# Kernel optimization log

Hardware: AMD Instinct MI355X
Metric: run time of the kernel (lower is better)

## Reference

```python
import jax, jax.numpy as jnp
import numpy as np

IN_DIM = 1024
HID = 256
OUT_DIM = 1000
NUM_BINS = 51
BATCH = 2048
N_LEGAL = 200


def setup_inputs() -> dict:
    key = jax.random.key(0)
    ks = jax.random.split(key, 12)
    s = lambda fan_in: 1.0 / np.sqrt(fan_in)
    u = lambda k, shp, b: jax.random.uniform(k, shp, jnp.float32, -b, b)
    return {
        "x": jax.random.normal(ks[0], (BATCH, IN_DIM), jnp.float32),
        # weights stored as [in, out] (math-equivalent to torch Linear)
        "w_in": u(ks[1], (IN_DIM, HID), s(IN_DIM)),
        "b_in": u(ks[2], (HID,), s(IN_DIM)),
        "w_ah": u(ks[3], (HID, HID), s(HID)),
        "b_ah": u(ks[4], (HID,), s(HID)),
        "w_ao": u(ks[5], (HID, OUT_DIM * NUM_BINS), s(HID)),
        "b_ao": u(ks[6], (OUT_DIM * NUM_BINS,), s(HID)),
        "w_vh": u(ks[7], (HID, HID), s(HID)),
        "b_vh": u(ks[8], (HID,), s(HID)),
        "w_vo": u(ks[9], (HID, NUM_BINS), s(HID)),
        "b_vo": u(ks[10], (NUM_BINS,), s(HID)),
        "v_range": jnp.linspace(-10.0, 10.0, NUM_BINS, dtype=jnp.float32),
        "possible_moves": jax.random.randint(ks[11], (BATCH, N_LEGAL), 0, OUT_DIM),
    }


def reference(x, w_in, b_in, w_ah, b_ah, w_ao, b_ao, w_vh, b_vh, w_vo, b_vo,
              v_range, possible_moves):
    B = x.shape[0]
    h = jax.nn.relu(x @ w_in + b_in)                       # [B, 256]
    adv_h = jax.nn.relu(h @ w_ah + b_ah)                   # [B, 256]
    val_h = jax.nn.relu(h @ w_vh + b_vh)                   # [B, 256]
    adv = (adv_h @ w_ao + b_ao).reshape(B, OUT_DIM, NUM_BINS)
    val = (val_h @ w_vo + b_vo).reshape(B, 1, NUM_BINS)
    q = val + adv - adv.mean(axis=1, keepdims=True)        # [B, A, bins]
    p = jnp.maximum(jax.nn.softmax(q, axis=2), 1e-5)       # softmax + clamp(min=1e-5)
    q_vals = jnp.sum(p * v_range, axis=2)                  # [B, A]
    # LegalSoftmax: per-row scatter of 1.0 at legal indices, vectorized
    mask = jnp.zeros((B, OUT_DIM), x.dtype).at[
        jnp.arange(B)[:, None], possible_moves].set(1.0)
    filtered = q_vals * mask
    # faithful to torch: any exact-zero entry (masked OR coincidental) -> -inf
    return jnp.where(filtered == 0, -jnp.inf, filtered)
```

## Files before the change

kernel.cpp:

```cpp
#include <hip/hip_runtime.h>
#include <cstdint>
#include <cstddef>

#define NB      2048
#define INDIM   1024
#define HID     256
#define NA      1000
#define BINS    51
#define NLEG    200
#define NPAIR   (NB*NLEG)
#define NBLK    256
#define PPB     (NPAIR/NBLK)

#define NEG_SENTINEL (-1.0e30f)

typedef float    f32x4  __attribute__((ext_vector_type(4)));
typedef __bf16   bf16x8 __attribute__((ext_vector_type(8)));
typedef unsigned short us8 __attribute__((ext_vector_type(8)));
typedef unsigned short us4 __attribute__((ext_vector_type(4)));
typedef unsigned long long u64x2 __attribute__((ext_vector_type(2)));

__device__ __forceinline__ unsigned short f2bf(float f) {
  union { float f; unsigned u; } v; v.f = f;
  return (unsigned short)((v.u + 0x7FFFu + ((v.u >> 16) & 1u)) >> 16);
}
__device__ __forceinline__ float bf2f(unsigned short h) {
  union { unsigned u; float f; } v; v.u = ((unsigned)h) << 16;
  return v.f;
}
__device__ __forceinline__ bf16x8 as_bf(us8 v) { return __builtin_bit_cast(bf16x8, v); }
__device__ __forceinline__ int imin(int a, int b) { return a < b ? a : b; }

__device__ __forceinline__ unsigned f2fp8x4(float a, float b, float c, float d) {
  int v = 0;
  v = __builtin_amdgcn_cvt_pk_fp8_f32(a, b, v, false);
  v = __builtin_amdgcn_cvt_pk_fp8_f32(c, d, v, true);
  return (unsigned)v;
}
__device__ __forceinline__ unsigned char f2fp8(float f) {
  int v = __builtin_amdgcn_cvt_pk_fp8_f32(f, 0.f, 0, false);
  return (unsigned char)(v & 0xff);
}
__device__ __forceinline__ float fp82f(unsigned char u) {
  return __builtin_amdgcn_cvt_f32_fp8((int)u, 0);
}

__global__ __launch_bounds__(256) void k_phase1(
    const float* __restrict__ w_ao, unsigned char* __restrict__ wp8,
    float* __restrict__ wmean_acc,
    const float* __restrict__ w_in, const float* __restrict__ w_ah,
    const float* __restrict__ w_vh,
    unsigned short* __restrict__ w_inT, unsigned short* __restrict__ w_ahT,
    unsigned short* __restrict__ w_vhT,
    float* __restrict__ out, const int* __restrict__ pm,
    int* __restrict__ hist, int* __restrict__ cnt,
    const float* __restrict__ x, unsigned short* __restrict__ x_bf) {
  __shared__ __align__(16) char smem[26240];
  int b = blockIdx.x, tid = threadIdx.x;
  if (b < 1000) {
    unsigned char* st = (unsigned char*)smem;
    int s = b & 7, a0 = (b >> 3) * 8;
    const float* wbase = w_ao + (size_t)(s * 32) * (NA * BINS) + a0 * BINS;
    for (int i = tid; i < 32 * 102; i += 256) {
      int r = i / 102, c4 = i - r * 102;
      float4 f = *(const float4*)(wbase + (size_t)r * (NA * BINS) + c4 * 4);
      *(unsigned*)(st + r * 420 + c4 * 4) =
          f2fp8x4(f.x * 16.f, f.y * 16.f, f.z * 16.f, f.w * 16.f);
    }
    __syncthreads();
    for (int i = tid; i < 32 * 51; i += 256) {
      int r = i / 51, j = i - r * 51;
      float s8 = 0.f;
#pragma unroll
      for (int aL = 0; aL < 8; aL++) s8 += fp82f(st[r * 420 + aL * 51 + j]);
      atomicAdd(&wmean_acc[(size_t)(s * 32 + r) * BINS + j], s8);
    }
    int t4 = (tid >> 6) & 3, l = tid & 63;
    int col = t4 * 16 + (l & 15), kg = l >> 4;
    for (int aL = 0; aL < 8; aL++) {
      unsigned lo = 0, hi = 0;
      if (col < BINS) {
        const unsigned char* p0 = st + (kg * 8) * 420 + aL * 51 + col;
        lo = (unsigned)p0[0] | ((unsigned)p0[420] << 8) |
             ((unsigned)p0[840] << 16) | ((unsigned)p0[1260] << 24);
        hi = (unsigned)p0[1680] | ((unsigned)p0[2100] << 8) |
             ((unsigned)p0[2520] << 16) | ((unsigned)p0[2940] << 24);
      }
      size_t fg = ((size_t)(a0 + aL) * 8 + s) * 4 + t4;
      uint2 v; v.x = lo; v.y = hi;
      *(uint2*)(wp8 + fg * 512 + (size_t)l * 8) = v;
    }
  } else if (b < 1884) {
    int bb = b - 1000;
    if (bb < 384) {
      float (*tile)[33] = (float(*)[33])smem;
      const float* w; unsigned short* wT; int K, N, kt, nt;
      if (bb < 256)      { w = w_in; wT = w_inT; K = INDIM; N = HID; kt = bb & 31;        nt = bb >> 5; }
      else if (bb < 320) { w = w_ah; wT = w_ahT; K = HID;   N = HID; kt = (bb - 256) & 7; nt = (bb - 256) >> 3; }
      else               { w = w_vh; wT = w_vhT; K = HID;   N = HID; kt = (bb - 320) & 7; nt = (bb - 320) >> 3; }
      int k0 = kt * 32, n0 = nt * 32;
      int cr = tid >> 5, cc = tid & 31;
#pragma unroll
      for (int it = 0; it < 4; it++)
        tile[cr + it * 8][cc] = w[(size_t)(k0 + cr + it * 8) * N + n0 + cc];
      __syncthreads();
#pragma unroll
      for (int it = 0; it < 4; it++)
        wT[(size_t)(n0 + cr + it * 8) * K + k0 + cc] = f2bf(tile[cc][cr + it * 8]);
    } else {
      int base = (bb - 384) * 1024 + tid;
      float4 v = {NEG_SENTINEL, NEG_SENTINEL, NEG_SENTINEL, NEG_SENTINEL};
#pragma unroll
      for (int it = 0; it < 4; it++) ((float4*)out)[base + it * 256] = v;
    }
  } else if (b < 2140) {
    int* lh = (int*)smem;
    int blk = b - 1884;
    for (int i = tid; i < NA; i += 256) lh[i] = 0;
    __syncthreads();
    int base = blk * PPB;
    for (int i = tid; i < PPB; i += 256) atomicAdd(&lh[pm[base + i]], 1);
    __syncthreads();
    for (int a = tid; a < NA; a += 256) {
      int v = lh[a];
      hist[a * NBLK + blk] = v;
      if (v) atomicAdd(&cnt[a], v);
    }
  } else {
    int bb = b - 2140;
    int base4 = bb * 1024 + tid;
#pragma unroll
    for (int it = 0; it < 4; it++) {
      float4 v = ((const float4*)x)[base4 + it * 256];
      us4 o;
      o[0] = f2bf(v.x); o[1] = f2bf(v.y); o[2] = f2bf(v.z); o[3] = f2bf(v.w);
      ((us4*)x_bf)[base4 + it * 256] = o;
    }
  }
}

__global__ __launch_bounds__(256) void k_phase2(
    int* __restrict__ hist, const int* __restrict__ cnt,
    const float* __restrict__ w_vo, const float* __restrict__ wmean_acc,
    const float* __restrict__ b_vo, const float* __restrict__ b_ao,
    unsigned short* __restrict__ Wc, float* __restrict__ bias_c,
    const unsigned short* __restrict__ x_bf, const unsigned short* __restrict__ w_inT,
    const float* __restrict__ b_in, unsigned short* __restrict__ h_bf,
    int* __restrict__ off) {
  int b = blockIdx.x, tid = threadIdx.x;
  if (b < 1000) {
    __shared__ int s[256];
    int a = b, t = tid;
    int v = hist[a * NBLK + t];
    s[t] = v;
    __syncthreads();
    for (int d = 1; d < 256; d <<= 1) {
      int u = (t >= d) ? s[t - d] : 0;
      __syncthreads();
      s[t] += u;
      __syncthreads();
    }
    hist[a * NBLK + t] = s[t] - v;
  } else if (b < 1064) {
    __shared__ float s[256];
    int n = b - 1000, t = tid;
    for (int k = t; k < 512; k += 256) {
      float v = 0.f;
      if (n < BINS)
        v = (k < 256) ? w_vo[(size_t)k * BINS + n]
                      : (-(0.001f / 16.f) * wmean_acc[(size_t)(k - 256) * BINS + n]);
      Wc[(size_t)n * 512 + k] = f2bf(v);
    }
    float acc = 0.f;
    if (n < BINS)
      for (int a = t; a < NA; a += 256) acc += b_ao[(size_t)a * BINS + n];
    s[t] = acc;
    __syncthreads();
    for (int d = 128; d > 0; d >>= 1) { if (t < d) s[t] += s[t + d]; __syncthreads(); }
    if (t == 0) bias_c[n] = (n < BINS) ? (b_vo[n] - 0.001f * s[0]) : 0.f;
  } else if (b < 1576) {
    int w = tid >> 6, l = tid & 63, la = l & 15, g = l >> 4;
    int idx = (b - 1064) * 4 + w;
    int m0 = (idx & 127) * 16, n0 = (idx >> 7) * 16;
    f32x4 acc = {0.f, 0.f, 0.f, 0.f};
    const us8* Bp = (const us8*)(w_inT + (size_t)(n0 + la) * INDIM) + g;
    const us8* Ap = (const us8*)(x_bf + (size_t)(m0 + la) * INDIM) + g;
#pragma unroll 8
    for (int s = 0; s < 32; s++)
      acc = __builtin_amdgcn_mfma_f32_16x16x32_bf16(as_bf(Ap[s * 4]), as_bf(Bp[s * 4]),
                                                    acc, 0, 0, 0);
    float bb = b_in[n0 + la];
#pragma unroll
    for (int r = 0; r < 4; r++) {
      float v = fmaxf(acc[r] + bb, 0.f);
      h_bf[(size_t)(m0 + g * 4 + r) * HID + n0 + la] = f2bf(v);
    }
  } else {
    __shared__ int s[256];
    int t = tid, i0 = 4 * t;
    int v0 = (i0     < NA) ? cnt[i0]     : 0;
    int v1 = (i0 + 1 < NA) ? cnt[i0 + 1] : 0;
    int v2 = (i0 + 2 < NA) ? cnt[i0 + 2] : 0;
    int v3 = (i0 + 3 < NA) ? cnt[i0 + 3] : 0;
    int sum = v0 + v1 + v2 + v3;
    s[t] = sum;
    __syncthreads();
    for (int d = 1; d < 256; d <<= 1) {
      int u = (t >= d) ? s[t - d] : 0;
      __syncthreads();
      s[t] += u;
      __syncthreads();
    }
    int excl = s[t] - sum;
    if (i0     < NA) off[i0]     = excl;
    if (i0 + 1 < NA) off[i0 + 1] = excl + v0;
    if (i0 + 2 < NA) off[i0 + 2] = excl + v0 + v1;
    if (i0 + 3 < NA) off[i0 + 3] = excl + v0 + v1 + v2;
  }
}

__global__ __launch_bounds__(256) void k_phase3(
    const unsigned short* __restrict__ h,
    const unsigned short* __restrict__ wA, const float* __restrict__ bA,
    unsigned char* __restrict__ Aext8, unsigned short* __restrict__ advh_bf,
    const unsigned short* __restrict__ wV, const float* __restrict__ bV,
    unsigned short* __restrict__ oV,
    const int* __restrict__ pm, const int* __restrict__ off,
    const int* __restrict__ hist, int* __restrict__ rows) {
  int b = blockIdx.x, tid = threadIdx.x;
  if (b < 1024) {
    int w = tid >> 6, l = tid & 63, la = l & 15, g = l >> 4;
    int idx = b * 4 + w;
    int m0 = (idx & 127) * 16;
    int ny = idx >> 7;
    int second = ny >> 4;
    int n0 = (ny & 15) * 16;
    const unsigned short* BT = second ? wV : wA;
    const float* bias = second ? bV : bA;
    f32x4 acc = {0.f, 0.f, 0.f, 0.f};
    const us8* Bp = (const us8*)(BT + (size_t)(n0 + la) * HID) + g;
    const us8* Ap = (const us8*)(h + (size_t)(m0 + la) * HID) + g;
#pragma unroll
    for (int s = 0; s < 8; s++)
      acc = __builtin_amdgcn_mfma_f32_16x16x32_bf16(as_bf(Ap[s * 4]), as_bf(Bp[s * 4]),
                                                    acc, 0, 0, 0);
    float bb = bias[n0 + la];
#pragma unroll
    for (int r = 0; r < 4; r++) {
      float v = fmaxf(acc[r] + bb, 0.f);
      size_t o = (size_t)(m0 + g * 4 + r) * HID + n0 + la;
      if (second) {
        oV[o] = f2bf(v);
      } else {
        advh_bf[o] = f2bf(v);
        Aext8[o] = f2fp8(v);
      }
    }
  } else {
    __shared__ int lc[NA];
    __shared__ int lbase[NA];
    int blk = b - 1024, t = tid;
    for (int i = t; i < NA; i += 256) {
      lc[i] = 0;
      lbase[i] = off[i] + hist[i * NBLK + blk];
    }
    __syncthreads();
    int base = blk * PPB;
    for (int i = t; i < PPB; i += 256) {
      int a = pm[base + i];
      int r = atomicAdd(&lc[a], 1);
      rows[lbase[a] + r] = (base + i) / NLEG;
    }
  }
}

__global__ __launch_bounds__(256) void k_phase4(
    const unsigned short* __restrict__ valh, const unsigned short* __restrict__ advh,
    const unsigned short* __restrict__ Wc, const float* __restrict__ bias_c,
    unsigned short* __restrict__ cbuf) {
  int b = blockIdx.x, tid = threadIdx.x;
  int w = tid >> 6, l = tid & 63, la = l & 15, g = l >> 4;
  int idx = b * 4 + w;
  int m0 = (idx & 127) * 16, n0 = (idx >> 7) * 16;
  f32x4 acc = {0.f, 0.f, 0.f, 0.f};
  const us8* Bp  = (const us8*)(Wc + (size_t)(n0 + la) * 512) + g;
  const us8* Ap1 = (const us8*)(valh + (size_t)(m0 + la) * HID) + g;
  const us8* Ap2 = (const us8*)(advh + (size_t)(m0 + la) * HID) + g;
#pragma unroll
  for (int s = 0; s < 8; s++)
    acc = __builtin_amdgcn_mfma_f32_16x16x32_bf16(as_bf(Ap1[s * 4]), as_bf(Bp[s * 4]),
                                                  acc, 0, 0, 0);
#pragma unroll
  for (int s = 0; s < 8; s++)
    acc = __builtin_amdgcn_mfma_f32_16x16x32_bf16(as_bf(Ap2[s * 4]), as_bf(Bp[(8 + s) * 4]),
                                                  acc, 0, 0, 0);
  float bb = bias_c[n0 + la];
#pragma unroll
  for (int r = 0; r < 4; r++)
    cbuf[(size_t)(m0 + g * 4 + r) * 64 + n0 + la] = f2bf(acc[r] + bb);
}

__global__ __launch_bounds__(256) void k_main_mfma(
    const unsigned char* __restrict__ Aext8,
    const unsigned short* __restrict__ cbuf,
    const unsigned char* __restrict__ wp8,
    const float* __restrict__ b_ao,
    const float* __restrict__ v_range,
    const int* __restrict__ cnt, const int* __restrict__ off,
    const int* __restrict__ rows,
    float* __restrict__ out) {
  __shared__ __align__(16) long long sB8[2048];
  int bx = blockIdx.x;
  int a = (bx & 7) * 125 + (bx >> 3);
  int count = cnt[a];
  int ntiles = (count + 15) >> 4;
  if ((int)(blockIdx.y * 4) >= ntiles) return;
  int tid = threadIdx.x;
  const u64x2* wpa = (const u64x2*)(wp8 + (size_t)a * 16384);
  for (int i = tid; i < 1024; i += 256) ((u64x2*)sB8)[i] = wpa[i];
  __syncthreads();

  int w = tid >> 6, l = tid & 63, la = l & 15, g = l >> 4;
  int base = off[a];

  float vr[4][4], bao[4][4];
#pragma unroll
  for (int t = 0; t < 4; t++)
#pragma unroll
    for (int r = 0; r < 4; r++) {
      int bin = t * 16 + g * 4 + r;
      bool vb = bin < BINS;
      vr[t][r]  = vb ? v_range[bin] : 0.f;
      bao[t][r] = vb ? b_ao[(size_t)a * BINS + bin] : NEG_SENTINEL;
    }

  us8 id0, id1;
#pragma unroll
  for (int j = 0; j < 8; j++) {
    id0[j] = (g * 8 + j == la)      ? (unsigned short)0x4180 : (unsigned short)0;
    id1[j] = (g * 8 + j == la + 16) ? (unsigned short)0x4180 : (unsigned short)0;
  }

  for (int tile = blockIdx.y * 4 + w; tile < ntiles; tile += 8) {
    int gi = tile * 16 + la;
    int rA = rows[base + imin(gi, count - 1)];
    const long long* Ap = (const long long*)(Aext8 + (size_t)rA * HID) + g;
    const us8* Cp = (const us8*)(cbuf + (size_t)rA * 64) + g;
    f32x4 acc[4];
#pragma unroll
    for (int t = 0; t < 4; t++) acc[t] = (f32x4){0.f, 0.f, 0.f, 0.f};
#pragma unroll
    for (int s = 0; s < 8; s++) {
      long long a8 = Ap[s * 4];
#pragma unroll
      for (int t = 0; t < 4; t++)
        acc[t] = __builtin_amdgcn_mfma_f32_16x16x32_fp8_fp8(
            sB8[(s * 4 + t) * 64 + l], a8, acc[t], 0, 0, 0);
    }
    {
      us8 c0 = Cp[0], c1 = Cp[4];
      acc[0] = __builtin_amdgcn_mfma_f32_16x16x32_bf16(as_bf(id0), as_bf(c0), acc[0], 0, 0, 0);
      acc[1] = __builtin_amdgcn_mfma_f32_16x16x32_bf16(as_bf(id1), as_bf(c0), acc[1], 0, 0, 0);
      acc[2] = __builtin_amdgcn_mfma_f32_16x16x32_bf16(as_bf(id0), as_bf(c1), acc[2], 0, 0, 0);
      acc[3] = __builtin_amdgcn_mfma_f32_16x16x32_bf16(as_bf(id1), as_bf(c1), acc[3], 0, 0, 0);
    }
    float e[4][4], S = 0.f;
#pragma unroll
    for (int t = 0; t < 4; t++)
#pragma unroll
      for (int r = 0; r < 4; r++) {
        float q = fmaf(acc[t][r], 0.0625f, bao[t][r]);
        float ev = __expf(q);
        e[t][r] = ev;
        S += ev;
      }
    S += __shfl_xor(S, 16);
    S += __shfl_xor(S, 32);
    float inv = 1.f / S;
    float qv = 0.f;
#pragma unroll
    for (int t = 0; t < 4; t++)
#pragma unroll
      for (int r = 0; r < 4; r++)
        qv = fmaf(fmaxf(e[t][r] * inv, 1e-5f), vr[t][r], qv);
    qv += __shfl_xor(qv, 16);
    qv += __shfl_xor(qv, 32);
    if (g == 0 && gi < count)
      out[(size_t)rA * NA + a] = (qv == 0.f) ? NEG_SENTINEL : qv;
  }
}

extern "C" void kernel_launch(void* const* d_in, const int* in_sizes, int n_in,
                              void* d_out, int out_size, void* d_ws, size_t ws_size,
                              hipStream_t stream) {
  (void)in_sizes; (void)n_in; (void)out_size; (void)ws_size;
  const float* x     = (const float*)d_in[0];
  const float* w_in  = (const float*)d_in[1];
  const float* b_in  = (const float*)d_in[2];
  const float* w_ah  = (const float*)d_in[3];
  const float* b_ah  = (const float*)d_in[4];
  const float* w_ao  = (const float*)d_in[5];
  const float* b_ao  = (const float*)d_in[6];
  const float* w_vh  = (const float*)d_in[7];
  const float* b_vh  = (const float*)d_in[8];
  const float* w_vo  = (const float*)d_in[9];
  const float* b_vo  = (const float*)d_in[10];
  const float* v_rng = (const float*)d_in[11];
  const int*   pm    = (const int*)d_in[12];
  float* out = (float*)d_out;

  char* p = (char*)d_ws;
  unsigned char*  wp8     = (unsigned char*)p;  p += (size_t)NA * 32 * 512;
  unsigned char*  Aext8   = (unsigned char*)p;  p += (size_t)NB * HID;
  unsigned short* cbuf    = (unsigned short*)p; p += (size_t)NB * 64 * 2;
  unsigned short* h_bf    = (unsigned short*)p; p += (size_t)NB * HID * 2;
  unsigned short* advh_bf = (unsigned short*)p; p += (size_t)NB * HID * 2;
  unsigned short* valh_bf = (unsigned short*)p; p += (size_t)NB * HID * 2;
  unsigned short* w_inT   = (unsigned short*)p; p += (size_t)HID * INDIM * 2;
  unsigned short* w_ahT   = (unsigned short*)p; p += (size_t)HID * HID * 2;
  unsigned short* w_vhT   = (unsigned short*)p; p += (size_t)HID * HID * 2;
  unsigned short* Wc      = (unsigned short*)p; p += (size_t)64 * 512 * 2;
  unsigned short* x_bf    = (unsigned short*)p; p += (size_t)NB * INDIM * 2;
  float* bias_c = (float*)p; p += 64 * 4;
  float* wmean  = (float*)p; p += 13056 * 4;
  int* cnt  = (int*)p; p += NA * 4;
  int* off  = (int*)p; p += NA * 4;
  int* hist = (int*)p; p += (size_t)NA * NBLK * 4;
  int* rows = (int*)p; p += (size_t)NPAIR * 4 + 256;

  hipMemsetAsync(wmean, 0, (13056 + NA) * sizeof(float), stream);

  k_phase1<<<2652, 256, 0, stream>>>(w_ao, wp8, wmean, w_in, w_ah, w_vh,
                                     w_inT, w_ahT, w_vhT, out, pm, hist, cnt,
                                     x, x_bf);
  k_phase2<<<1577, 256, 0, stream>>>(hist, cnt, w_vo, wmean, b_vo, b_ao,
                                     Wc, bias_c, x_bf, w_inT, b_in, h_bf, off);
  k_phase3<<<1280, 256, 0, stream>>>(h_bf, w_ahT, b_ah, Aext8, advh_bf,
                                     w_vhT, b_vh, valh_bf, pm, off, hist, rows);
  k_phase4<<<128, 256, 0, stream>>>(valh_bf, advh_bf, Wc, bias_c, cbuf);
  k_main_mfma<<<dim3(1000, 2), 256, 0, stream>>>(Aext8, cbuf, wp8, b_ao, v_rng,
                                                 cnt, off, rows, out);
}
```

Before: 207.6 us.

## Split w_ao packing across phases and hold packed weights in registers in main kernel

```diff
diff --git a/kernel.cpp b/kernel.cpp
--- a/kernel.cpp
+++ b/kernel.cpp
@@ -43,6 +43,43 @@
 }
 __device__ __forceinline__ float fp82f(unsigned char u) {
   return __builtin_amdgcn_cvt_f32_fp8((int)u, 0);
+}
+
+__device__ __forceinline__ void pack_body(
+    int s, int a0, char* smem, int tid,
+    const float* __restrict__ w_ao, unsigned char* __restrict__ wp8,
+    float* __restrict__ wmean_acc) {
+  unsigned char* st = (unsigned char*)smem;
+  const float* wbase = w_ao + (size_t)(s * 32) * (NA * BINS) + a0 * BINS;
+  for (int i = tid; i < 32 * 102; i += 256) {
+    int r = i / 102, c4 = i - r * 102;
+    float4 f = *(const float4*)(wbase + (size_t)r * (NA * BINS) + c4 * 4);
+    *(unsigned*)(st + r * 420 + c4 * 4) =
+        f2fp8x4(f.x * 16.f, f.y * 16.f, f.z * 16.f, f.w * 16.f);
+  }
+  __syncthreads();
+  for (int i = tid; i < 32 * 51; i += 256) {
+    int r = i / 51, j = i - r * 51;
+    float s8 = 0.f;
+#pragma unroll
+    for (int aL = 0; aL < 8; aL++) s8 += fp82f(st[r * 420 + aL * 51 + j]);
+    atomicAdd(&wmean_acc[(size_t)(s * 32 + r) * BINS + j], s8);
+  }
+  int t4 = (tid >> 6) & 3, l = tid & 63;
+  int col = t4 * 16 + (l & 15), kg = l >> 4;
+  for (int aL = 0; aL < 8; aL++) {
+    unsigned lo = 0, hi = 0;
+    if (col < BINS) {
+      const unsigned char* p0 = st + (kg * 8) * 420 + aL * 51 + col;
+      lo = (unsigned)p0[0] | ((unsigned)p0[420] << 8) |
+           ((unsigned)p0[840] << 16) | ((unsigned)p0[1260] << 24);
+      hi = (unsigned)p0[1680] | ((unsigned)p0[2100] << 8) |
+           ((unsigned)p0[2520] << 16) | ((unsigned)p0[2940] << 24);
+    }
+    size_t fg = ((size_t)(a0 + aL) * 8 + s) * 4 + t4;
+    uint2 v; v.x = lo; v.y = hi;
+    *(uint2*)(wp8 + fg * 512 + (size_t)l * 8) = v;
+  }
 }
 
 __global__ __launch_bounds__(256) void k_phase1(
@@ -55,67 +92,34 @@
     float* __restrict__ out, const int* __restrict__ pm,
     int* __restrict__ hist, int* __restrict__ cnt,
     const float* __restrict__ x, unsigned short* __restrict__ x_bf) {
-  __shared__ __align__(16) char smem[26240];
+  __shared__ __align__(16) char smem[13440];
   int b = blockIdx.x, tid = threadIdx.x;
-  if (b < 1000) {
-    unsigned char* st = (unsigned char*)smem;
-    int s = b & 7, a0 = (b >> 3) * 8;
-    const float* wbase = w_ao + (size_t)(s * 32) * (NA * BINS) + a0 * BINS;
-    for (int i = tid; i < 32 * 102; i += 256) {
-      int r = i / 102, c4 = i - r * 102;
-      float4 f = *(const float4*)(wbase + (size_t)r * (NA * BINS) + c4 * 4);
-      *(unsigned*)(st + r * 420 + c4 * 4) =
-          f2fp8x4(f.x * 16.f, f.y * 16.f, f.z * 16.f, f.w * 16.f);
-    }
-    __syncthreads();
-    for (int i = tid; i < 32 * 51; i += 256) {
-      int r = i / 51, j = i - r * 51;
-      float s8 = 0.f;
-#pragma unroll
-      for (int aL = 0; aL < 8; aL++) s8 += fp82f(st[r * 420 + aL * 51 + j]);
-      atomicAdd(&wmean_acc[(size_t)(s * 32 + r) * BINS + j], s8);
-    }
-    int t4 = (tid >> 6) & 3, l = tid & 63;
-    int col = t4 * 16 + (l & 15), kg = l >> 4;
-    for (int aL = 0; aL < 8; aL++) {
-      unsigned lo = 0, hi = 0;
-      if (col < BINS) {
-        const unsigned char* p0 = st + (kg * 8) * 420 + aL * 51 + col;
-        lo = (unsigned)p0[0] | ((unsigned)p0[420] << 8) |
-             ((unsigned)p0[840] << 16) | ((unsigned)p0[1260] << 24);
-        hi = (unsigned)p0[1680] | ((unsigned)p0[2100] << 8) |
-             ((unsigned)p0[2520] << 16) | ((unsigned)p0[2940] << 24);
-      }
-      size_t fg = ((size_t)(a0 + aL) * 8 + s) * 4 + t4;
-      uint2 v; v.x = lo; v.y = hi;
-      *(uint2*)(wp8 + fg * 512 + (size_t)l * 8) = v;
-    }
-  } else if (b < 1884) {
-    int bb = b - 1000;
-    if (bb < 384) {
-      float (*tile)[33] = (float(*)[33])smem;
-      const float* w; unsigned short* wT; int K, N, kt, nt;
-      if (bb < 256)      { w = w_in; wT = w_inT; K = INDIM; N = HID; kt = bb & 31;        nt = bb >> 5; }
-      else if (bb < 320) { w = w_ah; wT = w_ahT; K = HID;   N = HID; kt = (bb - 256) & 7; nt = (bb - 256) >> 3; }
-      else               { w = w_vh; wT = w_vhT; K = HID;   N = HID; kt = (bb - 320) & 7; nt = (bb - 320) >> 3; }
-      int k0 = kt * 32, n0 = nt * 32;
-      int cr = tid >> 5, cc = tid & 31;
-#pragma unroll
-      for (int it = 0; it < 4; it++)
-        tile[cr + it * 8][cc] = w[(size_t)(k0 + cr + it * 8) * N + n0 + cc];
-      __syncthreads();
-#pragma unroll
-      for (int it = 0; it < 4; it++)
-        wT[(size_t)(n0 + cr + it * 8) * K + k0 + cc] = f2bf(tile[cc][cr + it * 8]);
-    } else {
-      int base = (bb - 384) * 1024 + tid;
-      float4 v = {NEG_SENTINEL, NEG_SENTINEL, NEG_SENTINEL, NEG_SENTINEL};
-#pragma unroll
-      for (int it = 0; it < 4; it++) ((float4*)out)[base + it * 256] = v;
-    }
-  } else if (b < 2140) {
+  if (b < 500) {
+    pack_body(b & 3, (b >> 2) * 8, smem, tid, w_ao, wp8, wmean_acc);
+  } else if (b < 884) {
+    int bb = b - 500;
+    float (*tile)[33] = (float(*)[33])smem;
+    const float* w; unsigned short* wT; int K, N, kt, nt;
+    if (bb < 256)      { w = w_in; wT = w_inT; K = INDIM; N = HID; kt = bb & 31;        nt = bb >> 5; }
+    else if (bb < 320) { w = w_ah; wT = w_ahT; K = HID;   N = HID; kt = (bb - 256) & 7; nt = (bb - 256) >> 3; }
+    else               { w = w_vh; wT = w_vhT; K = HID;   N = HID; kt = (bb - 320) & 7; nt = (bb - 320) >> 3; }
+    int k0 = kt * 32, n0 = nt * 32;
+    int cr = tid >> 5, cc = tid & 31;
+#pragma unroll
+    for (int it = 0; it < 4; it++)
+      tile[cr + it * 8][cc] = w[(size_t)(k0 + cr + it * 8) * N + n0 + cc];
+    __syncthreads();
+#pragma unroll
+    for (int it = 0; it < 4; it++)
+      wT[(size_t)(n0 + cr + it * 8) * K + k0 + cc] = f2bf(tile[cc][cr + it * 8]);
+  } else if (b < 1384) {
+    int base = (b - 884) * 1024 + tid;
+    float4 v = {NEG_SENTINEL, NEG_SENTINEL, NEG_SENTINEL, NEG_SENTINEL};
+#pragma unroll
+    for (int it = 0; it < 4; it++) ((float4*)out)[base + it * 256] = v;
+  } else if (b < 1640) {
     int* lh = (int*)smem;
-    int blk = b - 1884;
+    int blk = b - 1384;
     for (int i = tid; i < NA; i += 256) lh[i] = 0;
     __syncthreads();
     int base = blk * PPB;
@@ -127,8 +131,7 @@
       if (v) atomicAdd(&cnt[a], v);
     }
   } else {
-    int bb = b - 2140;
-    int base4 = bb * 1024 + tid;
+    int base4 = (b - 1640) * 1024 + tid;
 #pragma unroll
     for (int it = 0; it < 4; it++) {
       float4 v = ((const float4*)x)[base4 + it * 256];
@@ -140,17 +143,19 @@
 }
 
 __global__ __launch_bounds__(256) void k_phase2(
+    const float* __restrict__ w_ao, unsigned char* __restrict__ wp8,
+    float* __restrict__ wmean_acc,
     int* __restrict__ hist, const int* __restrict__ cnt,
-    const float* __restrict__ w_vo, const float* __restrict__ wmean_acc,
-    const float* __restrict__ b_vo, const float* __restrict__ b_ao,
-    unsigned short* __restrict__ Wc, float* __restrict__ bias_c,
     const unsigned short* __restrict__ x_bf, const unsigned short* __restrict__ w_inT,
     const float* __restrict__ b_in, unsigned short* __restrict__ h_bf,
     int* __restrict__ off) {
+  __shared__ __align__(16) char smem[13440];
   int b = blockIdx.x, tid = threadIdx.x;
-  if (b < 1000) {
-    __shared__ int s[256];
-    int a = b, t = tid;
+  if (b < 500) {
+    pack_body(4 + (b & 3), (b >> 2) * 8, smem, tid, w_ao, wp8, wmean_acc);
+  } else if (b < 1500) {
+    int* s = (int*)smem;
+    int a = b - 500, t = tid;
     int v = hist[a * NBLK + t];
     s[t] = v;
     __syncthreads();
@@ -161,26 +166,9 @@
       __syncthreads();
     }
     hist[a * NBLK + t] = s[t] - v;
-  } else if (b < 1064) {
-    __shared__ float s[256];
-    int n = b - 1000, t = tid;
-    for (int k = t; k < 512; k += 256) {
-      float v = 0.f;
-      if (n < BINS)
-        v = (k < 256) ? w_vo[(size_t)k * BINS + n]
-                      : (-(0.001f / 16.f) * wmean_acc[(size_t)(k - 256) * BINS + n]);
-      Wc[(size_t)n * 512 + k] = f2bf(v);
-    }
-    float acc = 0.f;
-    if (n < BINS)
-      for (int a = t; a < NA; a += 256) acc += b_ao[(size_t)a * BINS + n];
-    s[t] = acc;
-    __syncthreads();
-    for (int d = 128; d > 0; d >>= 1) { if (t < d) s[t] += s[t + d]; __syncthreads(); }
-    if (t == 0) bias_c[n] = (n < BINS) ? (b_vo[n] - 0.001f * s[0]) : 0.f;
-  } else if (b < 1576) {
+  } else if (b < 2012) {
     int w = tid >> 6, l = tid & 63, la = l & 15, g = l >> 4;
-    int idx = (b - 1064) * 4 + w;
+    int idx = (b - 1500) * 4 + w;
     int m0 = (idx & 127) * 16, n0 = (idx >> 7) * 16;
     f32x4 acc = {0.f, 0.f, 0.f, 0.f};
     const us8* Bp = (const us8*)(w_inT + (size_t)(n0 + la) * INDIM) + g;
@@ -196,7 +184,7 @@
       h_bf[(size_t)(m0 + g * 4 + r) * HID + n0 + la] = f2bf(v);
     }
   } else {
-    __shared__ int s[256];
+    int* s = (int*)smem;
     int t = tid, i0 = 4 * t;
     int v0 = (i0     < NA) ? cnt[i0]     : 0;
     int v1 = (i0 + 1 < NA) ? cnt[i0 + 1] : 0;
@@ -226,7 +214,13 @@
     const unsigned short* __restrict__ wV, const float* __restrict__ bV,
     unsigned short* __restrict__ oV,
     const int* __restrict__ pm, const int* __restrict__ off,
-    const int* __restrict__ hist, int* __restrict__ rows) {
+    const int* __restrict__ hist, int* __restrict__ rows,
+    const float* __restrict__ w_vo, const float* __restrict__ wmean_acc,
+    const float* __restrict__ b_vo, const float* __restrict__ b_ao,
+    unsigned short* __restrict__ Wc, float* __restrict__ bias_c) {
+  __shared__ int lc[NA];
+  __shared__ int lbase[NA];
+  __shared__ float sred[256];
   int b = blockIdx.x, tid = threadIdx.x;
   if (b < 1024) {
     int w = tid >> 6, l = tid & 63, la = l & 15, g = l >> 4;
@@ -256,9 +250,7 @@
         Aext8[o] = f2fp8(v);
       }
     }
-  } else {
-    __shared__ int lc[NA];
-    __shared__ int lbase[NA];
+  } else if (b < 1280) {
     int blk = b - 1024, t = tid;
     for (int i = t; i < NA; i += 256) {
       lc[i] = 0;
@@ -271,6 +263,22 @@
       int r = atomicAdd(&lc[a], 1);
       rows[lbase[a] + r] = (base + i) / NLEG;
     }
+  } else {
+    int n = b - 1280, t = tid;
+    for (int k = t; k < 512; k += 256) {
+      float v = 0.f;
+      if (n < BINS)
+        v = (k < 256) ? w_vo[(size_t)k * BINS + n]
+                      : (-(0.001f / 16.f) * wmean_acc[(size_t)(k - 256) * BINS + n]);
+      Wc[(size_t)n * 512 + k] = f2bf(v);
+    }
+    float acc = 0.f;
+    if (n < BINS)
+      for (int a = t; a < NA; a += 256) acc += b_ao[(size_t)a * BINS + n];
+    sred[t] = acc;
+    __syncthreads();
+    for (int d = 128; d > 0; d >>= 1) { if (t < d) sred[t] += sred[t + d]; __syncthreads(); }
+    if (t == 0) bias_c[n] = (n < BINS) ? (b_vo[n] - 0.001f * sred[0]) : 0.f;
   }
 }
 
@@ -300,7 +308,7 @@
     cbuf[(size_t)(m0 + g * 4 + r) * 64 + n0 + la] = f2bf(acc[r] + bb);
 }
 
-__global__ __launch_bounds__(256) void k_main_mfma(
+__global__ __launch_bounds__(256, 3) void k_main_mfma(
     const unsigned char* __restrict__ Aext8,
     const unsigned short* __restrict__ cbuf,
     const unsigned char* __restrict__ wp8,
@@ -309,69 +317,69 @@
     const int* __restrict__ cnt, const int* __restrict__ off,
     const int* __restrict__ rows,
     float* __restrict__ out) {
-  __shared__ __align__(16) long long sB8[2048];
   int bx = blockIdx.x;
   int a = (bx & 7) * 125 + (bx >> 3);
   int count = cnt[a];
+  if (count <= 0) return;
   int ntiles = (count + 15) >> 4;
-  if ((int)(blockIdx.y * 4) >= ntiles) return;
   int tid = threadIdx.x;
-  const u64x2* wpa = (const u64x2*)(wp8 + (size_t)a * 16384);
-  for (int i = tid; i < 1024; i += 256) ((u64x2*)sB8)[i] = wpa[i];
-  __syncthreads();
-
   int w = tid >> 6, l = tid & 63, la = l & 15, g = l >> 4;
+
+  const long long* wpa = (const long long*)(wp8 + (size_t)a * 16384) + l;
+  long long b8[32];
+#pragma unroll
+  for (int f = 0; f < 32; f++) b8[f] = wpa[f * 64];
+
   int base = off[a];
 
-  float vr[4][4], bao[4][4];
+  float vr[16], bao[16];
 #pragma unroll
   for (int t = 0; t < 4; t++)
 #pragma unroll
     for (int r = 0; r < 4; r++) {
       int bin = t * 16 + g * 4 + r;
       bool vb = bin < BINS;
-      vr[t][r]  = vb ? v_range[bin] : 0.f;
-      bao[t][r] = vb ? b_ao[(size_t)a * BINS + bin] : NEG_SENTINEL;
-    }
-
-  us8 id0, id1;
-#pragma unroll
-  for (int j = 0; j < 8; j++) {
-    id0[j] = (g * 8 + j == la)      ? (unsigned short)0x4180 : (unsigned short)0;
-    id1[j] = (g * 8 + j == la + 16) ? (unsigned short)0x4180 : (unsigned short)0;
-  }
-
-  for (int tile = blockIdx.y * 4 + w; tile < ntiles; tile += 8) {
-    int gi = tile * 16 + la;
-    int rA = rows[base + imin(gi, count - 1)];
+      vr[t * 4 + r]  = vb ? v_range[bin] : 0.f;
+      bao[t * 4 + r] = vb ? b_ao[(size_t)a * BINS + bin] : NEG_SENTINEL;
+    }
+
+  int rAq[8];
+#pragma unroll
+  for (int i = 0; i < 8; i++) {
+    int t = w + i * 4;
+    rAq[i] = rows[base + imin(t * 16 + la, count - 1)];
+  }
+
+  auto body = [&](int tile, int rA) {
     const long long* Ap = (const long long*)(Aext8 + (size_t)rA * HID) + g;
-    const us8* Cp = (const us8*)(cbuf + (size_t)rA * 64) + g;
+    us4 cq[4];
+#pragma unroll
+    for (int t = 0; t < 4; t++)
+      cq[t] = *(const us4*)(cbuf + (size_t)rA * 64 + t * 16 + g * 4);
+    long long a8[8];
+#pragma unroll
+    for (int s = 0; s < 8; s++) a8[s] = Ap[s * 4];
     f32x4 acc[4];
 #pragma unroll
     for (int t = 0; t < 4; t++) acc[t] = (f32x4){0.f, 0.f, 0.f, 0.f};
+    __builtin_amdgcn_s_setprio(1);
 #pragma unroll
     for (int s = 0; s < 8; s++) {
-      long long a8 = Ap[s * 4];
 #pragma unroll
       for (int t = 0; t < 4; t++)
         acc[t] = __builtin_amdgcn_mfma_f32_16x16x32_fp8_fp8(
-            sB8[(s * 4 + t) * 64 + l], a8, acc[t], 0, 0, 0);
-    }
-    {
-      us8 c0 = Cp[0], c1 = Cp[4];
-      acc[0] = __builtin_amdgcn_mfma_f32_16x16x32_bf16(as_bf(id0), as_bf(c0), acc[0], 0, 0, 0);
-      acc[1] = __builtin_amdgcn_mfma_f32_16x16x32_bf16(as_bf(id1), as_bf(c0), acc[1], 0, 0, 0);
-      acc[2] = __builtin_amdgcn_mfma_f32_16x16x32_bf16(as_bf(id0), as_bf(c1), acc[2], 0, 0, 0);
-      acc[3] = __builtin_amdgcn_mfma_f32_16x16x32_bf16(as_bf(id1), as_bf(c1), acc[3], 0, 0, 0);
-    }
-    float e[4][4], S = 0.f;
+            b8[s * 4 + t], a8[s], acc[t], 0, 0, 0);
+    }
+    __builtin_amdgcn_s_setprio(0);
+    float e[16], S = 0.f;
 #pragma unroll
     for (int t = 0; t < 4; t++)
 #pragma unroll
       for (int r = 0; r < 4; r++) {
-        float q = fmaf(acc[t][r], 0.0625f, bao[t][r]);
+        float cb = bf2f(cq[t][r]) + bao[t * 4 + r];
+        float q = fmaf(acc[t][r], 0.0625f, cb);
         float ev = __expf(q);
-        e[t][r] = ev;
+        e[t * 4 + r] = ev;
         S += ev;
       }
     S += __shfl_xor(S, 16);
@@ -379,14 +387,23 @@
     float inv = 1.f / S;
     float qv = 0.f;
 #pragma unroll
-    for (int t = 0; t < 4; t++)
-#pragma unroll
-      for (int r = 0; r < 4; r++)
-        qv = fmaf(fmaxf(e[t][r] * inv, 1e-5f), vr[t][r], qv);
+    for (int j = 0; j < 16; j++)
+      qv = fmaf(fmaxf(e[j] * inv, 1e-5f), vr[j], qv);
     qv += __shfl_xor(qv, 16);
     qv += __shfl_xor(qv, 32);
+    int gi = tile * 16 + la;
     if (g == 0 && gi < count)
       out[(size_t)rA * NA + a] = (qv == 0.f) ? NEG_SENTINEL : qv;
+  };
+
+#pragma unroll
+  for (int i = 0; i < 8; i++) {
+    int tile = w + i * 4;
+    if (tile < ntiles) body(tile, rAq[i]);
+  }
+  for (int tile = 32 + w; tile < ntiles; tile += 4) {
+    int rA = rows[base + imin(tile * 16 + la, count - 1)];
+    body(tile, rA);
   }
 }
 
@@ -430,14 +447,15 @@
 
   hipMemsetAsync(wmean, 0, (13056 + NA) * sizeof(float), stream);
 
-  k_phase1<<<2652, 256, 0, stream>>>(w_ao, wp8, wmean, w_in, w_ah, w_vh,
+  k_phase1<<<2152, 256, 0, stream>>>(w_ao, wp8, wmean, w_in, w_ah, w_vh,
                                      w_inT, w_ahT, w_vhT, out, pm, hist, cnt,
                                      x, x_bf);
-  k_phase2<<<1577, 256, 0, stream>>>(hist, cnt, w_vo, wmean, b_vo, b_ao,
-                                     Wc, bias_c, x_bf, w_inT, b_in, h_bf, off);
-  k_phase3<<<1280, 256, 0, stream>>>(h_bf, w_ahT, b_ah, Aext8, advh_bf,
-                                     w_vhT, b_vh, valh_bf, pm, off, hist, rows);
+  k_phase2<<<2013, 256, 0, stream>>>(w_ao, wp8, wmean, hist, cnt,
+                                     x_bf, w_inT, b_in, h_bf, off);
+  k_phase3<<<1344, 256, 0, stream>>>(h_bf, w_ahT, b_ah, Aext8, advh_bf,
+                                     w_vhT, b_vh, valh_bf, pm, off, hist, rows,
+                                     w_vo, wmean, b_vo, b_ao, Wc, bias_c);
   k_phase4<<<128, 256, 0, stream>>>(valh_bf, advh_bf, Wc, bias_c, cbuf);
-  k_main_mfma<<<dim3(1000, 2), 256, 0, stream>>>(Aext8, cbuf, wp8, b_ao, v_rng,
-                                                 cnt, off, rows, out);
-}
+  k_main_mfma<<<1000, 256, 0, stream>>>(Aext8, cbuf, wp8, b_ao, v_rng,
+                                        cnt, off, rows, out);
+}
```

Result: slower. 217.4 us (+4.7%).
